# Kernel tuning notes

Measured on AMD Instinct MI355X. Metric: run time of the kernel, lower is better.

The kernel has to match this reference:

```python
import jax, jax.numpy as jnp
import numpy as np

NUM_GRAPHS = 100
NODES_PER_GRAPH = 400
UND_EDGES_PER_GRAPH = 5000  # -> 10000 directed edges per graph
UNITS = 64


def setup_inputs() -> dict:
    rng = np.random.default_rng(0)
    g = np.repeat(np.arange(NUM_GRAPHS), UND_EDGES_PER_GRAPH)
    src_l = rng.integers(0, NODES_PER_GRAPH, g.shape[0])
    dst_l = rng.integers(0, NODES_PER_GRAPH, g.shape[0])
    # avoid self loops (molecular graphs have none by default)
    dst_l = np.where(dst_l == src_l, (dst_l + 1) % NODES_PER_GRAPH, dst_l)
    src = (g * NODES_PER_GRAPH + src_l).astype(np.int32)
    dst = (g * NODES_PER_GRAPH + dst_l).astype(np.int32)
    # both directions, as produced by molecular graph encoders
    edge_src = jnp.asarray(np.concatenate([src, dst]))
    edge_dst = jnp.asarray(np.concatenate([dst, src]))
    E = edge_src.shape[0]
    num_nodes = NUM_GRAPHS * NODES_PER_GRAPH
    graph_indicator = jnp.asarray(
        np.repeat(np.arange(NUM_GRAPHS), NODES_PER_GRAPH).astype(np.int32))
    key = jax.random.key(0)
    k1, k2 = jax.random.split(key)
    edge_feature = jax.random.normal(k1, (E, UNITS), dtype=jnp.float32)
    W = jax.random.normal(k2, (2 * UNITS, UNITS), dtype=jnp.float32) * 0.005
    b = jnp.zeros((UNITS,), dtype=jnp.float32)
    return {"edge_feature": edge_feature, "edge_src": edge_src,
            "edge_dst": edge_dst, "graph_indicator": graph_indicator,
            "num_nodes": num_nodes, "W": W, "b": b}


def _reverse_edge_features(edge_feature, edge_src, edge_dst, num_nodes):
    # For each edge i, sum of edge_feature[j] over all j with
    # (src_j, dst_j) == (dst_i, src_i). Node ids are disjoint across
    # subgraphs, so a global (src,dst) key match is equivalent to the
    # per-subgraph match done by the original tf.map_fn version.
    E = edge_feature.shape[0]
    key = edge_src * num_nodes + edge_dst          # fits int32 for N<=46k
    rev = edge_dst * num_nodes + edge_src
    perm = jnp.argsort(key)
    sk = key[perm]
    # group duplicate keys (multi-edges) and sum their features
    new_grp = jnp.concatenate(
        [jnp.zeros((1,), sk.dtype), (sk[1:] != sk[:-1]).astype(sk.dtype)])
    gid = jnp.cumsum(new_grp)                      # [E] group id per sorted edge
    group_sum = jax.ops.segment_sum(edge_feature[perm], gid, num_segments=E)
    pos = jnp.clip(jnp.searchsorted(sk, rev), 0, E - 1)
    match = sk[pos] == rev
    return jnp.where(match[:, None], group_sum[gid[pos]], 0.0)


def reference(edge_feature, edge_src, edge_dst, graph_indicator, num_nodes, W, b):
    # message step: aggregate incoming edge states at each node, gather back
    # to each edge's source node, subtract the reverse edge's own state
    agg = jax.ops.segment_sum(edge_feature, edge_dst, num_segments=num_nodes)
    message = agg[edge_src] - _reverse_edge_features(
        edge_feature, edge_src, edge_dst, num_nodes)
    # update step: Dense(relu) on concat([prev_state, message])
    h = jnp.concatenate([edge_feature, message], axis=1)
    return jax.nn.relu(h @ W + b)
```

## Files before the change

kernel.cpp:

```cpp
#include <hip/hip_runtime.h>
#include <cstdint>
#include <cstddef>

#define TBL_LOG 19
static constexpr unsigned TBL = 1u << TBL_LOG;
static constexpr unsigned HASH_MUL = 2654435761u;

typedef __attribute__((ext_vector_type(8))) short short8;
typedef __attribute__((ext_vector_type(4))) float floatx4;

union U4S8 { uint4 u; short8 s; };

__device__ inline unsigned bf16rn(float x) {
    unsigned u = __float_as_uint(x);
    return (u + 0x7FFFu + ((u >> 16) & 1u)) >> 16;
}
__device__ inline unsigned pk2(float a, float b) {
    return bf16rn(a) | (bf16rn(b) << 16);
}

__global__ void wpack_kernel(const float* __restrict__ W, uint4* __restrict__ wsW) {
    const int lane = threadIdx.x;
    const int n = lane & 15, q = lane >> 4;
    for (int s = 0; s < 4; ++s)
        for (int t = 0; t < 4; ++t) {
            unsigned dw[4];
#pragma unroll
            for (int jj = 0; jj < 4; ++jj) {
                float a = W[(32 * s + 8 * q + 2 * jj) * 64 + 16 * t + n];
                float b = W[(32 * s + 8 * q + 2 * jj + 1) * 64 + 16 * t + n];
                dw[jj] = pk2(a, b);
            }
            wsW[(s * 4 + t) * 64 + lane] = make_uint4(dw[0], dw[1], dw[2], dw[3]);
        }
}

__global__ void build_hash_kernel(const int* __restrict__ esrc,
                                  const int* __restrict__ edst,
                                  int* __restrict__ heads,
                                  int* __restrict__ nxt,
                                  int E, unsigned NN) {
    int e = blockIdx.x * blockDim.x + threadIdx.x;
    if (e >= E) return;
    unsigned key = (unsigned)esrc[e] * NN + (unsigned)edst[e];
    unsigned b = (key * HASH_MUL) >> (32 - TBL_LOG);
    nxt[e] = atomicExch(&heads[b], e);
}

__global__ void hist_kernel(const int* __restrict__ edst, int* __restrict__ cnt, int E) {
    int e = blockIdx.x * blockDim.x + threadIdx.x;
    if (e < E) atomicAdd(&cnt[edst[e]], 1);
}

__global__ void scan_kernel(int* __restrict__ cnt, int* __restrict__ off, int NN, int E) {
    __shared__ int sd[1024];
    const int t = threadIdx.x;
    const int chunk = (NN + 1023) >> 10;
    const int lo = t * chunk, hi = min(lo + chunk, NN);
    int local = 0;
    for (int i = lo; i < hi; ++i) local += cnt[i];
    sd[t] = local;
    __syncthreads();
    for (int s = 1; s < 1024; s <<= 1) {
        int v = (t >= s) ? sd[t - s] : 0;
        __syncthreads();
        sd[t] += v;
        __syncthreads();
    }
    int run = sd[t] - local;
    for (int i = lo; i < hi; ++i) {
        int c = cnt[i];
        off[i] = run;
        cnt[i] = run;
        run += c;
    }
    if (t == 0) off[NN] = E;
}

__global__ void scatter_kernel(const int* __restrict__ edst, int* __restrict__ cursor,
                               int* __restrict__ csr, int E) {
    int e = blockIdx.x * blockDim.x + threadIdx.x;
    if (e >= E) return;
    int slot = atomicAdd(&cursor[edst[e]], 1);
    csr[slot] = e;
}

__global__ __launch_bounds__(256)
void agg_csr_kernel(const float* __restrict__ feat, const int* __restrict__ csr,
                    const int* __restrict__ off, float* __restrict__ agg, int NN) {
    const int wid = (blockIdx.x * blockDim.x + threadIdx.x) >> 6;
    const int lane = threadIdx.x & 63;
    if (wid >= NN) return;
    const int i0 = off[wid], i1 = off[wid + 1];
    float acc = 0.f;
    int i = i0;
    for (; i + 4 <= i1; i += 4) {
        int c0 = csr[i], c1 = csr[i + 1], c2 = csr[i + 2], c3 = csr[i + 3];
        float a0 = feat[((long long)c0 << 6) + lane];
        float a1 = feat[((long long)c1 << 6) + lane];
        float a2 = feat[((long long)c2 << 6) + lane];
        float a3 = feat[((long long)c3 << 6) + lane];
        acc += (a0 + a1) + (a2 + a3);
    }
    for (; i < i1; ++i) acc += feat[((long long)csr[i] << 6) + lane];
    agg[((long long)wid << 6) + lane] = acc;
}

__global__ __launch_bounds__(256, 2)
void fused_kernel(const float* __restrict__ feat,
                  const int* __restrict__ esrc,
                  const int* __restrict__ edst,
                  const float* __restrict__ agg,
                  const int* __restrict__ heads,
                  const int* __restrict__ nxt,
                  const uint4* __restrict__ wsW,
                  const float* __restrict__ bias,
                  float* __restrict__ out,
                  int E, unsigned NN) {
    __shared__ unsigned lds_h[64 * 68];
    const int tid = threadIdx.x;
    const int lane = tid & 63;
    const int n = lane & 15;
    const int q = lane >> 4;
    const long long base = (long long)blockIdx.x * 64;

    short8 wf[4][4];
#pragma unroll
    for (int s = 0; s < 4; ++s)
#pragma unroll
        for (int t = 0; t < 4; ++t) {
            U4S8 cvt;
            cvt.u = wsW[(s * 4 + t) * 64 + lane];
            wf[s][t] = cvt.s;
        }
    float bv[4];
#pragma unroll
    for (int t = 0; t < 4; ++t) bv[t] = bias[16 * t + n];

    const int el = tid >> 2;
    const int p = tid & 3;
    const long long e = base + el;
    float4 f0, f1, f2, f3, m0, m1, m2, m3;
    if (e < (long long)E) {
        const float4* fp = (const float4*)(feat + (e << 6) + 16 * p);
        f0 = fp[0]; f1 = fp[1]; f2 = fp[2]; f3 = fp[3];
        const int s = esrc[e], d = edst[e];
        const float4* ap = (const float4*)(agg + ((long long)s << 6) + 16 * p);
        m0 = ap[0]; m1 = ap[1]; m2 = ap[2]; m3 = ap[3];
        const unsigned rk = (unsigned)d * NN + (unsigned)s;
        int cur = heads[(rk * HASH_MUL) >> (32 - TBL_LOG)];
        while (cur >= 0) {
            if ((unsigned)esrc[cur] * NN + (unsigned)edst[cur] == rk) {
                const float4* rp = (const float4*)(feat + ((long long)cur << 6) + 16 * p);
                float4 r0 = rp[0], r1 = rp[1], r2 = rp[2], r3 = rp[3];
                m0.x -= r0.x; m0.y -= r0.y; m0.z -= r0.z; m0.w -= r0.w;
                m1.x -= r1.x; m1.y -= r1.y; m1.z -= r1.z; m1.w -= r1.w;
                m2.x -= r2.x; m2.y -= r2.y; m2.z -= r2.z; m2.w -= r2.w;
                m3.x -= r3.x; m3.y -= r3.y; m3.z -= r3.z; m3.w -= r3.w;
            }
            cur = nxt[cur];
        }
    } else {
        f0 = f1 = f2 = f3 = make_float4(0.f, 0.f, 0.f, 0.f);
        m0 = m1 = m2 = m3 = make_float4(0.f, 0.f, 0.f, 0.f);
    }
    unsigned* row = &lds_h[el * 68];
    *(uint4*)(row + 8 * p) =
        make_uint4(pk2(f0.x, f0.y), pk2(f0.z, f0.w), pk2(f1.x, f1.y), pk2(f1.z, f1.w));
    *(uint4*)(row + 8 * p + 4) =
        make_uint4(pk2(f2.x, f2.y), pk2(f2.z, f2.w), pk2(f3.x, f3.y), pk2(f3.z, f3.w));
    *(uint4*)(row + 32 + 8 * p) =
        make_uint4(pk2(m0.x, m0.y), pk2(m0.z, m0.w), pk2(m1.x, m1.y), pk2(m1.z, m1.w));
    *(uint4*)(row + 32 + 8 * p + 4) =
        make_uint4(pk2(m2.x, m2.y), pk2(m2.z, m2.w), pk2(m3.x, m3.y), pk2(m3.z, m3.w));
    __syncthreads();

    const int w = tid >> 6;
    floatx4 acc[4];
#pragma unroll
    for (int t = 0; t < 4; ++t) acc[t] = (floatx4){0.f, 0.f, 0.f, 0.f};
#pragma unroll
    for (int s = 0; s < 4; ++s) {
        U4S8 a;
        a.u = *(const uint4*)&lds_h[(16 * w + n) * 68 + 16 * s + 4 * q];
#pragma unroll
        for (int t = 0; t < 4; ++t)
            acc[t] = __builtin_amdgcn_mfma_f32_16x16x32_bf16(a.s, wf[s][t], acc[t], 0, 0, 0);
    }

    const long long rbase = base + 16 * w + 4 * q;
#pragma unroll
    for (int t = 0; t < 4; ++t)
#pragma unroll
        for (int r = 0; r < 4; ++r) {
            long long rr = rbase + r;
            if (rr < (long long)E) {
                float v = acc[t][r] + bv[t];
                out[(rr << 6) + 16 * t + n] = v > 0.f ? v : 0.f;
            }
        }
}

extern "C" void kernel_launch(void* const* d_in, const int* in_sizes, int n_in,
                              void* d_out, int out_size, void* d_ws, size_t ws_size,
                              hipStream_t stream) {
    const float* feat = (const float*)d_in[0];
    const int*   esrc = (const int*)d_in[1];
    const int*   edst = (const int*)d_in[2];
    const float* W    = (const float*)d_in[5];
    const float* bias = (const float*)d_in[6];
    float* out = (float*)d_out;

    const int E  = in_sizes[1];
    const int NN = in_sizes[3];

    char* ws = (char*)d_ws;
    size_t o = 0;
    auto alloc = [&](size_t bytes) { void* p = ws + o; o = (o + bytes + 15) & ~(size_t)15; return p; };
    float* agg   = (float*)alloc((size_t)NN * 64 * sizeof(float));
    int*   heads = (int*)alloc((size_t)TBL * sizeof(int));
    int*   nxt   = (int*)alloc((size_t)E * sizeof(int));
    int*   cnt   = (int*)alloc((size_t)NN * sizeof(int));
    int*   off   = (int*)alloc((size_t)(NN + 1) * sizeof(int));
    int*   csr   = (int*)alloc((size_t)E * sizeof(int));
    uint4* wsW   = (uint4*)alloc((size_t)16 * 64 * sizeof(uint4));

    hipMemsetAsync(cnt, 0, (size_t)NN * sizeof(int), stream);
    hipMemsetAsync(heads, 0xFF, (size_t)TBL * sizeof(int), stream);

    const int eb = (E + 255) / 256;
    wpack_kernel<<<1, 64, 0, stream>>>(W, wsW);
    hist_kernel<<<eb, 256, 0, stream>>>(edst, cnt, E);
    scan_kernel<<<1, 1024, 0, stream>>>(cnt, off, NN, E);
    scatter_kernel<<<eb, 256, 0, stream>>>(edst, cnt, csr, E);
    build_hash_kernel<<<eb, 256, 0, stream>>>(esrc, edst, heads, nxt, E, (unsigned)NN);
    agg_csr_kernel<<<(NN + 3) / 4, 256, 0, stream>>>(feat, csr, off, agg, NN);
    fused_kernel<<<(E + 63) / 64, 256, 0, stream>>>(
        feat, esrc, edst, agg, heads, nxt, wsW, bias, out, E, (unsigned)NN);
}
```

Baseline: 897.0 us.

## Replace chained hash with open-addressing table and precompute reverse edge ids

Replaces the linked-list hash of edge keys with a 64-bit open-addressing table. A new pass resolves each edge's unique reverse-edge index ahead of time, so the fused kernel usually does one direct feature load instead of walking a chain. The fused kernel also maps each block to edges i and i+E/2 when E is a multiple of 64, so an edge and its likely reverse are handled by the same block for better cache locality. The cost is a larger 16MB table to memset and probe, plus an extra kernel launch.

```diff
diff --git a/kernel.cpp b/kernel.cpp
--- a/kernel.cpp
+++ b/kernel.cpp
@@ -2,8 +2,9 @@
 #include <cstdint>
 #include <cstddef>
 
-#define TBL_LOG 19
-static constexpr unsigned TBL = 1u << TBL_LOG;
+#define OA_LOG 21
+static constexpr unsigned OA_SLOTS = 1u << OA_LOG;
+static constexpr unsigned OA_MASK  = OA_SLOTS - 1;
 static constexpr unsigned HASH_MUL = 2654435761u;
 
 typedef __attribute__((ext_vector_type(8))) short short8;
@@ -33,18 +34,6 @@
             }
             wsW[(s * 4 + t) * 64 + lane] = make_uint4(dw[0], dw[1], dw[2], dw[3]);
         }
-}
-
-__global__ void build_hash_kernel(const int* __restrict__ esrc,
-                                  const int* __restrict__ edst,
-                                  int* __restrict__ heads,
-                                  int* __restrict__ nxt,
-                                  int E, unsigned NN) {
-    int e = blockIdx.x * blockDim.x + threadIdx.x;
-    if (e >= E) return;
-    unsigned key = (unsigned)esrc[e] * NN + (unsigned)edst[e];
-    unsigned b = (key * HASH_MUL) >> (32 - TBL_LOG);
-    nxt[e] = atomicExch(&heads[b], e);
 }
 
 __global__ void hist_kernel(const int* __restrict__ edst, int* __restrict__ cnt, int E) {
@@ -106,13 +95,46 @@
     agg[((long long)wid << 6) + lane] = acc;
 }
 
+__global__ void build_oa_kernel(const int* __restrict__ esrc,
+                                const int* __restrict__ edst,
+                                unsigned long long* __restrict__ tbl,
+                                int E, unsigned NN) {
+    int e = blockIdx.x * blockDim.x + threadIdx.x;
+    if (e >= E) return;
+    unsigned k = (unsigned)esrc[e] * NN + (unsigned)edst[e];
+    unsigned long long mine = ((unsigned long long)(unsigned)e << 32) | (unsigned long long)k;
+    unsigned s = (k * HASH_MUL) >> (32 - OA_LOG);
+    const unsigned long long EMPTY = ~0ull;
+    while (atomicCAS(&tbl[s], EMPTY, mine) != EMPTY)
+        s = (s + 1) & OA_MASK;
+}
+
+__global__ void mark_rev_kernel(const int* __restrict__ esrc,
+                                const int* __restrict__ edst,
+                                const unsigned long long* __restrict__ tbl,
+                                int* __restrict__ revid,
+                                int E, unsigned NN) {
+    int e = blockIdx.x * blockDim.x + threadIdx.x;
+    if (e >= E) return;
+    unsigned rk = (unsigned)edst[e] * NN + (unsigned)esrc[e];
+    unsigned s = (rk * HASH_MUL) >> (32 - OA_LOG);
+    int cnt = 0, idx = -1;
+    while (true) {
+        unsigned long long v = tbl[s];
+        if ((unsigned)v == 0xFFFFFFFFu) break;
+        if ((unsigned)v == rk) { ++cnt; idx = (int)(v >> 32); }
+        s = (s + 1) & OA_MASK;
+    }
+    revid[e] = (cnt == 1) ? idx : -1;
+}
+
 __global__ __launch_bounds__(256, 2)
 void fused_kernel(const float* __restrict__ feat,
                   const int* __restrict__ esrc,
                   const int* __restrict__ edst,
                   const float* __restrict__ agg,
-                  const int* __restrict__ heads,
-                  const int* __restrict__ nxt,
+                  const unsigned long long* __restrict__ tbl,
+                  const int* __restrict__ revid,
                   const uint4* __restrict__ wsW,
                   const float* __restrict__ bias,
                   float* __restrict__ out,
@@ -122,7 +144,9 @@
     const int lane = tid & 63;
     const int n = lane & 15;
     const int q = lane >> 4;
-    const long long base = (long long)blockIdx.x * 64;
+    const int g = blockIdx.x;
+    const long long H = (long long)(E >> 1);
+    const bool paired = (E & 63) == 0;
 
     short8 wf[4][4];
 #pragma unroll
@@ -139,27 +163,46 @@
 
     const int el = tid >> 2;
     const int p = tid & 3;
-    const long long e = base + el;
+    long long e;
+    if (paired) e = (long long)g * 32 + (el & 31) + (long long)(el >> 5) * H;
+    else        e = (long long)g * 64 + el;
+
     float4 f0, f1, f2, f3, m0, m1, m2, m3;
     if (e < (long long)E) {
         const float4* fp = (const float4*)(feat + (e << 6) + 16 * p);
         f0 = fp[0]; f1 = fp[1]; f2 = fp[2]; f3 = fp[3];
-        const int s = esrc[e], d = edst[e];
-        const float4* ap = (const float4*)(agg + ((long long)s << 6) + 16 * p);
+        const int s_ = esrc[e], d_ = edst[e];
+        const float4* ap = (const float4*)(agg + ((long long)s_ << 6) + 16 * p);
         m0 = ap[0]; m1 = ap[1]; m2 = ap[2]; m3 = ap[3];
-        const unsigned rk = (unsigned)d * NN + (unsigned)s;
-        int cur = heads[(rk * HASH_MUL) >> (32 - TBL_LOG)];
-        while (cur >= 0) {
-            if ((unsigned)esrc[cur] * NN + (unsigned)edst[cur] == rk) {
-                const float4* rp = (const float4*)(feat + ((long long)cur << 6) + 16 * p);
-                float4 r0 = rp[0], r1 = rp[1], r2 = rp[2], r3 = rp[3];
-                m0.x -= r0.x; m0.y -= r0.y; m0.z -= r0.z; m0.w -= r0.w;
-                m1.x -= r1.x; m1.y -= r1.y; m1.z -= r1.z; m1.w -= r1.w;
-                m2.x -= r2.x; m2.y -= r2.y; m2.z -= r2.z; m2.w -= r2.w;
-                m3.x -= r3.x; m3.y -= r3.y; m3.z -= r3.z; m3.w -= r3.w;
+
+        const int rid = revid[e];
+        float4 r0, r1, r2, r3;
+        if (rid >= 0) {
+            const float4* rp = (const float4*)(feat + ((long long)rid << 6) + 16 * p);
+            r0 = rp[0]; r1 = rp[1]; r2 = rp[2]; r3 = rp[3];
+        } else {
+            r0 = r1 = r2 = r3 = make_float4(0.f, 0.f, 0.f, 0.f);
+            const unsigned rk = (unsigned)d_ * NN + (unsigned)s_;
+            unsigned slot = (rk * HASH_MUL) >> (32 - OA_LOG);
+            while (true) {
+                unsigned long long v = tbl[slot];
+                if ((unsigned)v == 0xFFFFFFFFu) break;
+                if ((unsigned)v == rk) {
+                    const float4* rp =
+                        (const float4*)(feat + ((long long)(v >> 32) << 6) + 16 * p);
+                    float4 a0 = rp[0], a1 = rp[1], a2 = rp[2], a3 = rp[3];
+                    r0.x += a0.x; r0.y += a0.y; r0.z += a0.z; r0.w += a0.w;
+                    r1.x += a1.x; r1.y += a1.y; r1.z += a1.z; r1.w += a1.w;
+                    r2.x += a2.x; r2.y += a2.y; r2.z += a2.z; r2.w += a2.w;
+                    r3.x += a3.x; r3.y += a3.y; r3.z += a3.z; r3.w += a3.w;
+                }
+                slot = (slot + 1) & OA_MASK;
             }
-            cur = nxt[cur];
-        }
+        }
+        m0.x -= r0.x; m0.y -= r0.y; m0.z -= r0.z; m0.w -= r0.w;
+        m1.x -= r1.x; m1.y -= r1.y; m1.z -= r1.z; m1.w -= r1.w;
+        m2.x -= r2.x; m2.y -= r2.y; m2.z -= r2.z; m2.w -= r2.w;
+        m3.x -= r3.x; m3.y -= r3.y; m3.z -= r3.z; m3.w -= r3.w;
     } else {
         f0 = f1 = f2 = f3 = make_float4(0.f, 0.f, 0.f, 0.f);
         m0 = m1 = m2 = m3 = make_float4(0.f, 0.f, 0.f, 0.f);
@@ -188,17 +231,20 @@
             acc[t] = __builtin_amdgcn_mfma_f32_16x16x32_bf16(a.s, wf[s][t], acc[t], 0, 0, 0);
     }
 
-    const long long rbase = base + 16 * w + 4 * q;
-#pragma unroll
-    for (int t = 0; t < 4; ++t)
-#pragma unroll
-        for (int r = 0; r < 4; ++r) {
-            long long rr = rbase + r;
-            if (rr < (long long)E) {
+#pragma unroll
+    for (int r = 0; r < 4; ++r) {
+        const int rowi = 16 * w + 4 * q + r;
+        long long ee;
+        if (paired) ee = (long long)g * 32 + (rowi & 31) + (long long)(rowi >> 5) * H;
+        else        ee = (long long)g * 64 + rowi;
+        if (ee < (long long)E) {
+#pragma unroll
+            for (int t = 0; t < 4; ++t) {
                 float v = acc[t][r] + bv[t];
-                out[(rr << 6) + 16 * t + n] = v > 0.f ? v : 0.f;
+                out[(ee << 6) + 16 * t + n] = v > 0.f ? v : 0.f;
             }
         }
+    }
 }
 
 extern "C" void kernel_launch(void* const* d_in, const int* in_sizes, int n_in,
@@ -218,23 +264,24 @@
     size_t o = 0;
     auto alloc = [&](size_t bytes) { void* p = ws + o; o = (o + bytes + 15) & ~(size_t)15; return p; };
     float* agg   = (float*)alloc((size_t)NN * 64 * sizeof(float));
-    int*   heads = (int*)alloc((size_t)TBL * sizeof(int));
-    int*   nxt   = (int*)alloc((size_t)E * sizeof(int));
     int*   cnt   = (int*)alloc((size_t)NN * sizeof(int));
     int*   off   = (int*)alloc((size_t)(NN + 1) * sizeof(int));
     int*   csr   = (int*)alloc((size_t)E * sizeof(int));
+    unsigned long long* tbl = (unsigned long long*)alloc((size_t)OA_SLOTS * 8);
+    int*   revid = (int*)alloc((size_t)E * sizeof(int));
     uint4* wsW   = (uint4*)alloc((size_t)16 * 64 * sizeof(uint4));
 
     hipMemsetAsync(cnt, 0, (size_t)NN * sizeof(int), stream);
-    hipMemsetAsync(heads, 0xFF, (size_t)TBL * sizeof(int), stream);
+    hipMemsetAsync(tbl, 0xFF, (size_t)OA_SLOTS * 8, stream);
 
     const int eb = (E + 255) / 256;
     wpack_kernel<<<1, 64, 0, stream>>>(W, wsW);
     hist_kernel<<<eb, 256, 0, stream>>>(edst, cnt, E);
     scan_kernel<<<1, 1024, 0, stream>>>(cnt, off, NN, E);
     scatter_kernel<<<eb, 256, 0, stream>>>(edst, cnt, csr, E);
-    build_hash_kernel<<<eb, 256, 0, stream>>>(esrc, edst, heads, nxt, E, (unsigned)NN);
+    build_oa_kernel<<<eb, 256, 0, stream>>>(esrc, edst, tbl, E, (unsigned)NN);
+    mark_rev_kernel<<<eb, 256, 0, stream>>>(esrc, edst, tbl, revid, E, (unsigned)NN);
     agg_csr_kernel<<<(NN + 3) / 4, 256, 0, stream>>>(feat, csr, off, agg, NN);
     fused_kernel<<<(E + 63) / 64, 256, 0, stream>>>(
-        feat, esrc, edst, agg, heads, nxt, wsW, bias, out, E, (unsigned)NN);
-}
+        feat, esrc, edst, agg, tbl, revid, wsW, bias, out, E, (unsigned)NN);
+}
```

Result: faster. 838.5 us (-6.5%).
